# Performance work log

Hardware: AMD Instinct MI355X
Metric: run time of the kernel (lower is better)

The kernel has to match this reference:

```python
import jax, jax.numpy as jnp
import numpy as np

EPS = 1e-8


def setup_inputs() -> dict:
    key = jax.random.key(0)
    k1, k2 = jax.random.split(key)
    B, C, L = 16, 4, 4096
    K, S = 256, 128
    x = jax.random.normal(k1, (B, C, L), dtype=jnp.float32)
    shapelets = jax.random.normal(k2, (C, K, S), dtype=jnp.float32)
    return {"x": x, "shapelets": shapelets}


def reference(x, shapelets):
    # x: (B, C, L); shapelets: (C, K, S)
    B, C, L = x.shape
    _, K, S = shapelets.shape
    W = L - S + 1  # number of sliding windows

    # unfold: (B, C, W, S) sliding windows with stride 1
    idx = jnp.arange(W)[:, None] + jnp.arange(S)[None, :]  # (W, S)
    win = x[:, :, idx]  # (B, C, W, S)
    win = win / jnp.maximum(jnp.linalg.norm(win, axis=-1, keepdims=True), EPS)

    shp = shapelets / jnp.maximum(
        jnp.linalg.norm(shapelets, axis=-1, keepdims=True), EPS
    )  # (C, K, S)

    # pairwise dot products: (B, C, W, K)
    sim = jnp.einsum("bcws,cks->bcwk", win, shp)
    # sum over channels, keepdim, transpose(2,3), divide by n_dims
    sim = jnp.sum(sim, axis=1, keepdims=True) / C  # (B, 1, W, K)
    sim = jnp.transpose(sim, (0, 1, 3, 2))  # (B, 1, K, W)
    sim = jax.nn.relu(sim)
    # global max-pool over window positions -> (B, 1, K)
    return jnp.max(sim, axis=3)
```

## Files before the change

kernel.cpp:

```cpp
#include <hip/hip_runtime.h>
#include <hip/hip_bf16.h>

#define NB 16
#define NC 4
#define NL 4096
#define NK 256
#define NS 128
#define NW (NL - NS + 1)
#define WPB 128
#define NWT ((NW + WPB - 1) / WPB)
#define KPB 64
#define EPSF 1e-8f

typedef __attribute__((ext_vector_type(8))) short bf16x8;
typedef __attribute__((ext_vector_type(4))) float floatx4;

typedef __attribute__((address_space(3))) unsigned int* lds_ptr_t;
typedef const __attribute__((address_space(1))) unsigned int* gbl_ptr_t;

__device__ inline short f2bf(float f) {
    __hip_bfloat16 h = __float2bfloat16(f);
    short s;
    __builtin_memcpy(&s, &h, sizeof(short));
    return s;
}

__device__ inline void gload_lds16(const void* g, void* l) {
    __builtin_amdgcn_global_load_lds((gbl_ptr_t)g, (lds_ptr_t)l, 16, 0, 0);
}

__global__ __launch_bounds__(64)
void norm_shp_kernel(const float* __restrict__ shp, short* __restrict__ shpn) {
    int ck = blockIdx.x;
    int k = ck & (NK - 1);
    int lane = threadIdx.x;
    const float* p = shp + (size_t)ck * NS;
    float v0 = p[lane];
    float v1 = p[lane + 64];
    float ss = v0 * v0 + v1 * v1;
    #pragma unroll
    for (int o = 32; o > 0; o >>= 1) ss += __shfl_xor(ss, o, 64);
    float rn = 1.f / fmaxf(sqrtf(ss), EPSF);
    int s0 = lane, s1 = lane + 64;
    int d0 = ((((s0 >> 3) ^ (k & 15)) << 3) | (s0 & 7));
    int d1 = ((((s1 >> 3) ^ (k & 15)) << 3) | (s1 & 7));
    shpn[(size_t)ck * NS + d0] = f2bf(v0 * rn);
    shpn[(size_t)ck * NS + d1] = f2bf(v1 * rn);
}

__global__ __launch_bounds__(256, 2)
void mcs_main_kernel(const float* __restrict__ x,
                     const short* __restrict__ shpn,
                     float* __restrict__ out) {
    __shared__ bf16x8 bs[NC][KPB * 16];
    __shared__ alignas(16) short xcp[NC][4][264];
    __shared__ alignas(16) float scratch[NC][264];
    __shared__ float invw[NC][WPB];

    const int wt = blockIdx.x, kq = blockIdx.y, b = blockIdx.z;
    const int w0 = wt * WPB;
    const int tid = threadIdx.x;
    const int lane = tid & 63, wv = tid >> 6;

    {
        const char* gbase = (const char*)shpn + (size_t)(kq * KPB) * NS * 2;
        #pragma unroll
        for (int c = 0; c < NC; c++) {
            const char* gc = gbase + (size_t)c * NK * NS * 2;
            char* lc = (char*)&bs[c][0];
            #pragma unroll
            for (int i = 0; i < 4; i++) {
                int off = (wv * 4 + i) * 1024;
                gload_lds16(gc + off + lane * 16, lc + off);
            }
        }
    }

    float xv[NC];
    #pragma unroll
    for (int c = 0; c < NC; c++) {
        int g = w0 + tid;
        xv[c] = (g < NL) ? x[((size_t)b * NC + c) * NL + g] : 0.f;
    }
    #pragma unroll
    for (int c = 0; c < NC; c++) {
        short hv = f2bf(xv[c]);
        #pragma unroll
        for (int r = 0; r < 4; r++) {
            int o2 = tid - r;
            if (o2 >= 0) xcp[c][r][o2] = hv;
        }
        scratch[c][tid] = xv[c] * xv[c];
    }
    __syncthreads();

    {
        float4 v = *(const float4*)&scratch[wv][lane * 4];
        v.y += v.x; v.z += v.y; v.w += v.z;
        float tt = v.w;
        #pragma unroll
        for (int o = 1; o < 64; o <<= 1) {
            float u = __shfl_up(tt, o, 64);
            if (lane >= o) tt += u;
        }
        float excl = tt - v.w;
        v.x += excl; v.y += excl; v.z += excl; v.w += excl;
        *(float4*)&scratch[wv][lane * 4] = v;
    }
    __syncthreads();

    #pragma unroll
    for (int i = 0; i < 2; i++) {
        int idx = tid + 256 * i;
        int c = idx >> 7, o = idx & 127;
        float nn = scratch[c][o + 127] - (o ? scratch[c][o - 1] : 0.f);
        int w = w0 + o;
        invw[c][o] = (w < NW) ? 1.f / fmaxf(sqrtf(fmaxf(nn, 0.f)), EPSF) : 0.f;
    }
    __syncthreads();

    const int m = lane & 15, q = lane >> 4, r = m & 3;
    const int kh = wv & 1, wh = wv >> 1;

    floatx4 tot[4][2];
    #pragma unroll
    for (int mt = 0; mt < 4; mt++)
        #pragma unroll
        for (int kt = 0; kt < 2; kt++) tot[mt][kt] = (floatx4){0.f, 0.f, 0.f, 0.f};

    #pragma unroll
    for (int c = 0; c < NC; c++) {
        floatx4 part[4][2];
        #pragma unroll
        for (int s0 = 0; s0 < NS; s0 += 32) {
            bf16x8 a[4];
            #pragma unroll
            for (int mt = 0; mt < 4; mt++) {
                int ts = wh * 64 + mt * 16 + m + s0 + q * 8;
                const uint2* pp = (const uint2*)&xcp[c][r][ts - r];
                union { uint2 uu[2]; bf16x8 v; } cv;
                cv.uu[0] = pp[0]; cv.uu[1] = pp[1];
                a[mt] = cv.v;
            }
            int cc = (s0 >> 3) + q;
            #pragma unroll
            for (int kt = 0; kt < 2; kt++) {
                int k = kh * 32 + kt * 16 + m;
                bf16x8 bf = bs[c][(k << 4) | (cc ^ m)];
                #pragma unroll
                for (int mt = 0; mt < 4; mt++) {
                    part[mt][kt] = (s0 == 0)
                        ? __builtin_amdgcn_mfma_f32_16x16x32_bf16(
                              a[mt], bf, (floatx4){0.f, 0.f, 0.f, 0.f}, 0, 0, 0)
                        : __builtin_amdgcn_mfma_f32_16x16x32_bf16(
                              a[mt], bf, part[mt][kt], 0, 0, 0);
                }
            }
        }
        #pragma unroll
        for (int mt = 0; mt < 4; mt++) {
            const float4 iv = *(const float4*)&invw[c][wh * 64 + mt * 16 + q * 4];
            floatx4 ivv = (floatx4){iv.x, iv.y, iv.z, iv.w};
            #pragma unroll
            for (int kt = 0; kt < 2; kt++) tot[mt][kt] += ivv * part[mt][kt];
        }
    }

    #pragma unroll
    for (int kt = 0; kt < 2; kt++) {
        floatx4 v0 = tot[0][kt], v1 = tot[1][kt], v2 = tot[2][kt], v3 = tot[3][kt];
        float mx = fmaxf(fmaxf(fmaxf(v0.x, v0.y), fmaxf(v0.z, v0.w)),
                         fmaxf(fmaxf(v1.x, v1.y), fmaxf(v1.z, v1.w)));
        mx = fmaxf(mx, fmaxf(fmaxf(fmaxf(v2.x, v2.y), fmaxf(v2.z, v2.w)),
                             fmaxf(fmaxf(v3.x, v3.y), fmaxf(v3.z, v3.w))));
        mx = fmaxf(mx, __shfl_xor(mx, 16, 64));
        mx = fmaxf(mx, __shfl_xor(mx, 32, 64));
        if (lane < 16) scratch[wv][kt * 16 + lane] = mx;
    }
    __syncthreads();
    if (tid < 64) {
        int khh = tid >> 5, j = tid & 31;
        float v = fmaxf(scratch[khh][j], scratch[khh + 2][j]);
        v = fmaxf(v, 0.f) * 0.25f;
        int kg = kq * KPB + khh * 32 + j;
        atomicMax((int*)out + (size_t)b * NK + kg, __float_as_int(v));
    }
}

extern "C" void kernel_launch(void* const* d_in, const int* in_sizes, int n_in,
                              void* d_out, int out_size, void* d_ws, size_t ws_size,
                              hipStream_t stream) {
    (void)in_sizes; (void)n_in; (void)out_size; (void)ws_size;
    const float* x   = (const float*)d_in[0];
    const float* shp = (const float*)d_in[1];
    float* out = (float*)d_out;

    short* shpn = (short*)d_ws;

    norm_shp_kernel<<<NC * NK, 64, 0, stream>>>(shp, shpn);
    mcs_main_kernel<<<dim3(NWT, 4, NB), 256, 0, stream>>>(x, shpn, out);
}
```

Baseline: 80.75 us.

## Make main kernel persistent over four window tiles and prefetch next x tile

```diff
diff --git a/kernel.cpp b/kernel.cpp
--- a/kernel.cpp
+++ b/kernel.cpp
@@ -57,10 +57,11 @@
     __shared__ alignas(16) float scratch[NC][264];
     __shared__ float invw[NC][WPB];
 
-    const int wt = blockIdx.x, kq = blockIdx.y, b = blockIdx.z;
-    const int w0 = wt * WPB;
+    const int kq = blockIdx.x, slot = blockIdx.y;
     const int tid = threadIdx.x;
     const int lane = tid & 63, wv = tid >> 6;
+    const int m = lane & 15, q = lane >> 4, r = m & 3;
+    const int kh = wv & 1, wh = wv >> 1;
 
     {
         const char* gbase = (const char*)shpn + (size_t)(kq * KPB) * NS * 2;
@@ -77,113 +78,135 @@
     }
 
     float xv[NC];
-    #pragma unroll
-    for (int c = 0; c < NC; c++) {
-        int g = w0 + tid;
-        xv[c] = (g < NL) ? x[((size_t)b * NC + c) * NL + g] : 0.f;
+    {
+        int idx = slot * 4;
+        int wt = idx & 31, b = idx >> 5;
+        int g = wt * WPB + tid;
+        #pragma unroll
+        for (int c = 0; c < NC; c++)
+            xv[c] = (g < NL) ? x[((size_t)b * NC + c) * NL + g] : 0.f;
     }
-    #pragma unroll
-    for (int c = 0; c < NC; c++) {
-        short hv = f2bf(xv[c]);
-        #pragma unroll
-        for (int r = 0; r < 4; r++) {
-            int o2 = tid - r;
-            if (o2 >= 0) xcp[c][r][o2] = hv;
-        }
-        scratch[c][tid] = xv[c] * xv[c];
-    }
-    __syncthreads();
-
-    {
-        float4 v = *(const float4*)&scratch[wv][lane * 4];
-        v.y += v.x; v.z += v.y; v.w += v.z;
-        float tt = v.w;
-        #pragma unroll
-        for (int o = 1; o < 64; o <<= 1) {
-            float u = __shfl_up(tt, o, 64);
-            if (lane >= o) tt += u;
-        }
-        float excl = tt - v.w;
-        v.x += excl; v.y += excl; v.z += excl; v.w += excl;
-        *(float4*)&scratch[wv][lane * 4] = v;
-    }
-    __syncthreads();
-
-    #pragma unroll
-    for (int i = 0; i < 2; i++) {
-        int idx = tid + 256 * i;
-        int c = idx >> 7, o = idx & 127;
-        float nn = scratch[c][o + 127] - (o ? scratch[c][o - 1] : 0.f);
-        int w = w0 + o;
-        invw[c][o] = (w < NW) ? 1.f / fmaxf(sqrtf(fmaxf(nn, 0.f)), EPSF) : 0.f;
-    }
-    __syncthreads();
-
-    const int m = lane & 15, q = lane >> 4, r = m & 3;
-    const int kh = wv & 1, wh = wv >> 1;
-
-    floatx4 tot[4][2];
-    #pragma unroll
-    for (int mt = 0; mt < 4; mt++)
-        #pragma unroll
-        for (int kt = 0; kt < 2; kt++) tot[mt][kt] = (floatx4){0.f, 0.f, 0.f, 0.f};
-
-    #pragma unroll
-    for (int c = 0; c < NC; c++) {
-        floatx4 part[4][2];
-        #pragma unroll
-        for (int s0 = 0; s0 < NS; s0 += 32) {
-            bf16x8 a[4];
-            #pragma unroll
-            for (int mt = 0; mt < 4; mt++) {
-                int ts = wh * 64 + mt * 16 + m + s0 + q * 8;
-                const uint2* pp = (const uint2*)&xcp[c][r][ts - r];
-                union { uint2 uu[2]; bf16x8 v; } cv;
-                cv.uu[0] = pp[0]; cv.uu[1] = pp[1];
-                a[mt] = cv.v;
-            }
-            int cc = (s0 >> 3) + q;
-            #pragma unroll
-            for (int kt = 0; kt < 2; kt++) {
-                int k = kh * 32 + kt * 16 + m;
-                bf16x8 bf = bs[c][(k << 4) | (cc ^ m)];
+
+    for (int t = 0; t < 4; t++) {
+        const int idx = slot * 4 + t;
+        const int wt = idx & 31, b = idx >> 5;
+        const int w0 = wt * WPB;
+
+        #pragma unroll
+        for (int c = 0; c < NC; c++) {
+            short hv = f2bf(xv[c]);
+            #pragma unroll
+            for (int rr = 0; rr < 4; rr++) {
+                int o2 = tid - rr;
+                if (o2 >= 0) xcp[c][rr][o2] = hv;
+            }
+            scratch[c][tid] = xv[c] * xv[c];
+        }
+        __syncthreads();
+
+        {
+            float4 v = *(const float4*)&scratch[wv][lane * 4];
+            v.y += v.x; v.z += v.y; v.w += v.z;
+            float tt = v.w;
+            #pragma unroll
+            for (int o = 1; o < 64; o <<= 1) {
+                float u = __shfl_up(tt, o, 64);
+                if (lane >= o) tt += u;
+            }
+            float excl = tt - v.w;
+            v.x += excl; v.y += excl; v.z += excl; v.w += excl;
+            *(float4*)&scratch[wv][lane * 4] = v;
+        }
+        __syncthreads();
+
+        #pragma unroll
+        for (int i = 0; i < 2; i++) {
+            int ii = tid + 256 * i;
+            int c = ii >> 7, o = ii & 127;
+            float nn = scratch[c][o + 127] - (o ? scratch[c][o - 1] : 0.f);
+            int w = w0 + o;
+            invw[c][o] = (w < NW) ? 1.f / fmaxf(sqrtf(fmaxf(nn, 0.f)), EPSF)
+                                  : 0.f;
+        }
+        if (t == 0) asm volatile("s_waitcnt vmcnt(0)" ::: "memory");
+        __syncthreads();
+
+        if (t < 3) {
+            int idxn = idx + 1;
+            int wtn = idxn & 31, bn = idxn >> 5;
+            int g = wtn * WPB + tid;
+            #pragma unroll
+            for (int c = 0; c < NC; c++)
+                xv[c] = (g < NL) ? x[((size_t)bn * NC + c) * NL + g] : 0.f;
+        }
+
+        floatx4 tot[4][2];
+        #pragma unroll
+        for (int mt = 0; mt < 4; mt++)
+            #pragma unroll
+            for (int kt = 0; kt < 2; kt++)
+                tot[mt][kt] = (floatx4){0.f, 0.f, 0.f, 0.f};
+
+        #pragma unroll
+        for (int c = 0; c < NC; c++) {
+            floatx4 part[4][2];
+            #pragma unroll
+            for (int s0 = 0; s0 < NS; s0 += 32) {
+                bf16x8 a[4];
                 #pragma unroll
                 for (int mt = 0; mt < 4; mt++) {
-                    part[mt][kt] = (s0 == 0)
-                        ? __builtin_amdgcn_mfma_f32_16x16x32_bf16(
-                              a[mt], bf, (floatx4){0.f, 0.f, 0.f, 0.f}, 0, 0, 0)
-                        : __builtin_amdgcn_mfma_f32_16x16x32_bf16(
-                              a[mt], bf, part[mt][kt], 0, 0, 0);
+                    int ts = wh * 64 + mt * 16 + m + s0 + q * 8;
+                    const uint2* pp = (const uint2*)&xcp[c][r][ts - r];
+                    union { uint2 uu[2]; bf16x8 v; } cv;
+                    cv.uu[0] = pp[0]; cv.uu[1] = pp[1];
+                    a[mt] = cv.v;
                 }
-            }
-        }
-        #pragma unroll
-        for (int mt = 0; mt < 4; mt++) {
-            const float4 iv = *(const float4*)&invw[c][wh * 64 + mt * 16 + q * 4];
-            floatx4 ivv = (floatx4){iv.x, iv.y, iv.z, iv.w};
-            #pragma unroll
-            for (int kt = 0; kt < 2; kt++) tot[mt][kt] += ivv * part[mt][kt];
-        }
-    }
-
-    #pragma unroll
-    for (int kt = 0; kt < 2; kt++) {
-        floatx4 v0 = tot[0][kt], v1 = tot[1][kt], v2 = tot[2][kt], v3 = tot[3][kt];
-        float mx = fmaxf(fmaxf(fmaxf(v0.x, v0.y), fmaxf(v0.z, v0.w)),
-                         fmaxf(fmaxf(v1.x, v1.y), fmaxf(v1.z, v1.w)));
-        mx = fmaxf(mx, fmaxf(fmaxf(fmaxf(v2.x, v2.y), fmaxf(v2.z, v2.w)),
-                             fmaxf(fmaxf(v3.x, v3.y), fmaxf(v3.z, v3.w))));
-        mx = fmaxf(mx, __shfl_xor(mx, 16, 64));
-        mx = fmaxf(mx, __shfl_xor(mx, 32, 64));
-        if (lane < 16) scratch[wv][kt * 16 + lane] = mx;
-    }
-    __syncthreads();
-    if (tid < 64) {
-        int khh = tid >> 5, j = tid & 31;
-        float v = fmaxf(scratch[khh][j], scratch[khh + 2][j]);
-        v = fmaxf(v, 0.f) * 0.25f;
-        int kg = kq * KPB + khh * 32 + j;
-        atomicMax((int*)out + (size_t)b * NK + kg, __float_as_int(v));
+                int cc = (s0 >> 3) + q;
+                #pragma unroll
+                for (int kt = 0; kt < 2; kt++) {
+                    int k = kh * 32 + kt * 16 + m;
+                    bf16x8 bf = bs[c][(k << 4) | (cc ^ m)];
+                    #pragma unroll
+                    for (int mt = 0; mt < 4; mt++) {
+                        part[mt][kt] = (s0 == 0)
+                            ? __builtin_amdgcn_mfma_f32_16x16x32_bf16(
+                                  a[mt], bf, (floatx4){0.f,0.f,0.f,0.f}, 0,0,0)
+                            : __builtin_amdgcn_mfma_f32_16x16x32_bf16(
+                                  a[mt], bf, part[mt][kt], 0, 0, 0);
+                    }
+                }
+            }
+            #pragma unroll
+            for (int mt = 0; mt < 4; mt++) {
+                const float4 iv =
+                    *(const float4*)&invw[c][wh * 64 + mt * 16 + q * 4];
+                floatx4 ivv = (floatx4){iv.x, iv.y, iv.z, iv.w};
+                #pragma unroll
+                for (int kt = 0; kt < 2; kt++) tot[mt][kt] += ivv * part[mt][kt];
+            }
+        }
+
+        #pragma unroll
+        for (int kt = 0; kt < 2; kt++) {
+            floatx4 v0 = tot[0][kt], v1 = tot[1][kt],
+                    v2 = tot[2][kt], v3 = tot[3][kt];
+            float mx = fmaxf(fmaxf(fmaxf(v0.x, v0.y), fmaxf(v0.z, v0.w)),
+                             fmaxf(fmaxf(v1.x, v1.y), fmaxf(v1.z, v1.w)));
+            mx = fmaxf(mx, fmaxf(fmaxf(fmaxf(v2.x, v2.y), fmaxf(v2.z, v2.w)),
+                                 fmaxf(fmaxf(v3.x, v3.y), fmaxf(v3.z, v3.w))));
+            mx = fmaxf(mx, __shfl_xor(mx, 16, 64));
+            mx = fmaxf(mx, __shfl_xor(mx, 32, 64));
+            if (lane < 16) scratch[wv][kt * 16 + lane] = mx;
+        }
+        __syncthreads();
+        if (tid < 64) {
+            int khh = tid >> 5, j = tid & 31;
+            float v = fmaxf(scratch[khh][j], scratch[khh + 2][j]);
+            v = fmaxf(v, 0.f) * 0.25f;
+            int kg = kq * KPB + khh * 32 + j;
+            atomicMax((int*)out + (size_t)b * NK + kg, __float_as_int(v));
+        }
+        __syncthreads();
     }
 }
 
@@ -198,5 +221,5 @@
     short* shpn = (short*)d_ws;
 
     norm_shp_kernel<<<NC * NK, 64, 0, stream>>>(shp, shpn);
-    mcs_main_kernel<<<dim3(NWT, 4, NB), 256, 0, stream>>>(x, shpn, out);
-}
+    mcs_main_kernel<<<dim3(4, 128), 256, 0, stream>>>(x, shpn, out);
+}
```

After: 76.56 us. -5.2%, faster.
